# Performance work log

Measured on AMD Instinct MI355X. Metric: run time of the kernel, lower is better.

The kernel has to match this reference:

```python
import jax, jax.numpy as jnp
import numpy as np

B, CIN, H, W = 4, 1024, 64, 64
PLANES = 256
K = 3
DIL = 2
PAD = DIL * (K - 1) // 2  # = 2
EPS = 1e-5


def setup_inputs() -> dict:
    key = jax.random.key(0)
    ks = jax.random.split(key, 16)
    d = {}
    d['x'] = jax.random.normal(ks[0], (B, CIN, H, W), dtype=jnp.float32)
    # conv1: 1x1, inplanes->planes, no bias
    d['w1'] = jax.random.normal(ks[1], (PLANES, CIN), dtype=jnp.float32) * 0.02
    d['gamma1'] = jnp.ones((PLANES,), jnp.float32)
    d['beta1'] = jnp.zeros((PLANES,), jnp.float32)
    d['mean1'] = jax.random.normal(ks[2], (PLANES,), dtype=jnp.float32) * 0.1
    d['var1'] = jax.random.uniform(ks[3], (PLANES,), minval=0.5, maxval=1.5, dtype=jnp.float32)
    # deform_offset: 3x3 conv planes->18, with bias
    d['woff'] = jax.random.normal(ks[4], (18, PLANES, K, K), dtype=jnp.float32) * 0.01
    d['boff'] = jnp.zeros((18,), jnp.float32)
    # conv2 (deformable): 3x3 planes->planes, with bias
    d['w2'] = jax.random.normal(ks[5], (PLANES, PLANES, K, K), dtype=jnp.float32) * 0.02
    d['bconv2'] = jnp.zeros((PLANES,), jnp.float32)
    d['gamma2'] = jnp.ones((PLANES,), jnp.float32)
    d['beta2'] = jnp.zeros((PLANES,), jnp.float32)
    d['mean2'] = jax.random.normal(ks[6], (PLANES,), dtype=jnp.float32) * 0.1
    d['var2'] = jax.random.uniform(ks[7], (PLANES,), minval=0.5, maxval=1.5, dtype=jnp.float32)
    # conv3: 1x1 planes->planes*4, no bias
    d['w3'] = jax.random.normal(ks[8], (PLANES * 4, PLANES), dtype=jnp.float32) * 0.02
    d['gamma3'] = jnp.ones((PLANES * 4,), jnp.float32)
    d['beta3'] = jnp.zeros((PLANES * 4,), jnp.float32)
    d['mean3'] = jax.random.normal(ks[9], (PLANES * 4,), dtype=jnp.float32) * 0.1
    d['var3'] = jax.random.uniform(ks[10], (PLANES * 4,), minval=0.5, maxval=1.5, dtype=jnp.float32)
    return d


def _bn(x, gamma, beta, mean, var):
    # inference-mode BatchNorm over channel dim (NCHW)
    inv = jax.lax.rsqrt(var + EPS)
    return (x - mean[:, None, None]) * (inv * gamma)[:, None, None] + beta[:, None, None]


def _deform_conv(x, offset, w, b):
    # x: [B,C,H,W]; offset: [B,18,H,W] ordered (dy,dx) per kernel tap; w: [O,C,3,3]
    Bn, C, Hh, Ww = x.shape
    off = offset.reshape(Bn, K * K, 2, Hh, Ww)
    off_y, off_x = off[:, :, 0], off[:, :, 1]          # [B,9,H,W]
    kk = jnp.arange(K * K)
    base_y = (kk // K) * DIL - PAD                      # [9]
    base_x = (kk % K) * DIL - PAD
    ys = jnp.arange(Hh, dtype=x.dtype)
    xs = jnp.arange(Ww, dtype=x.dtype)
    py = base_y.astype(x.dtype)[None, :, None, None] + ys[None, None, :, None] + off_y
    px = base_x.astype(x.dtype)[None, :, None, None] + xs[None, None, None, :] + off_x

    def sample_one(img, py1, px1):
        # img [C,H,W]; py1/px1 [9,H,W] -> [C,9,H,W] bilinear with zero padding
        y0 = jnp.floor(py1)
        x0 = jnp.floor(px1)
        wy = py1 - y0
        wx = px1 - x0

        def gather(yc, xc):
            yi = yc.astype(jnp.int32)
            xi = xc.astype(jnp.int32)
            valid = ((yi >= 0) & (yi < Hh) & (xi >= 0) & (xi < Ww)).astype(img.dtype)
            yi = jnp.clip(yi, 0, Hh - 1)
            xi = jnp.clip(xi, 0, Ww - 1)
            return img[:, yi, xi] * valid[None]

        v00 = gather(y0, x0)
        v01 = gather(y0, x0 + 1)
        v10 = gather(y0 + 1, x0)
        v11 = gather(y0 + 1, x0 + 1)
        return (v00 * ((1 - wy) * (1 - wx))[None] + v01 * ((1 - wy) * wx)[None]
                + v10 * (wy * (1 - wx))[None] + v11 * (wy * wx)[None])

    sampled = jax.vmap(sample_one)(x, py, px)           # [B,C,9,H,W]
    out = jnp.einsum('bckhw,ock->bohw', sampled, w.reshape(w.shape[0], C, K * K))
    return out + b[None, :, None, None]


def reference(x, w1, gamma1, beta1, mean1, var1, woff, boff, w2, bconv2,
              gamma2, beta2, mean2, var2, w3, gamma3, beta3, mean3, var3):
    residual = x
    out = jnp.einsum('bchw,oc->bohw', x, w1)            # conv1 1x1
    out = jax.nn.relu(_bn(out, gamma1, beta1, mean1, var1))
    offset = jax.lax.conv_general_dilated(
        out, woff, window_strides=(1, 1), padding=((PAD, PAD), (PAD, PAD)),
        rhs_dilation=(DIL, DIL), dimension_numbers=('NCHW', 'OIHW', 'NCHW'))
    offset = offset + boff[None, :, None, None]
    out = _deform_conv(out, offset, w2, bconv2)
    out = jax.nn.relu(_bn(out, gamma2, beta2, mean2, var2))
    out = jnp.einsum('bchw,oc->bohw', out, w3)          # conv3 1x1
    out = _bn(out, gamma3, beta3, mean3, var3)
    return jax.nn.relu(out + residual)
```

## Files before the change

### kernel.cpp

```cpp
#include <hip/hip_runtime.h>

#define EPS_BN 1e-5f

typedef __bf16 bf16x8 __attribute__((ext_vector_type(8)));
typedef float f32x4 __attribute__((ext_vector_type(4)));

__device__ __forceinline__ unsigned short f2bf(float f) {
  union { float f; unsigned u; } v; v.f = f;
  unsigned r = v.u + 0x7fffu + ((v.u >> 16) & 1u);
  return (unsigned short)(r >> 16);
}
__device__ __forceinline__ float bf2f(unsigned short h) {
  union { unsigned u; float f; } v; v.u = ((unsigned)h) << 16;
  return v.f;
}

__global__ __launch_bounds__(256) void prep_all(
    const float* __restrict__ w1, const float* __restrict__ w2, const float* __restrict__ woff,
    const float* __restrict__ w3,
    const float* g1, const float* b1, const float* m1, const float* v1,
    const float* g2, const float* b2, const float* m2, const float* v2, const float* bconv2,
    const float* g3, const float* b3, const float* m3, const float* v3,
    unsigned short* __restrict__ w1b, unsigned short* __restrict__ w2r,
    uint4* __restrict__ act1Pz, unsigned short* __restrict__ wob,
    unsigned short* __restrict__ w3b, float* __restrict__ shift3,
    float* s1, float* h1, float* s2, float* h2) {
  int bid = blockIdx.x, tid = threadIdx.x;
  if (bid < 1024) {
    int i = bid * 256 + tid;
    w1b[i] = f2bf(w1[i]);
  } else if (bid < 3328) {
    int i = (bid - 1024) * 256 + tid;
    int o = i / 2304, r = i % 2304;
    int kk = r / 256, c = r % 256;
    w2r[i] = f2bf(w2[(size_t)o * 2304 + c * 9 + kk]);
  } else if (bid < 5640) {
    int i = (bid - 3328) * 256 + tid;
    if (i < 591872) act1Pz[i] = uint4{0, 0, 0, 0};
  } else if (bid < 5928) {
    int i = (bid - 5640) * 256 + tid;
    int o = i / 2304, r = i % 2304;
    int kk = r / 256, c = r % 256;
    wob[i] = (o < 18) ? f2bf(woff[(size_t)o * 2304 + c * 9 + kk]) : (unsigned short)0;
  } else if (bid < 6952) {
    int i = (bid - 5928) * 256 + tid;
    int o = i >> 8;
    float sc = rsqrtf(v3[o] + EPS_BN) * g3[o];
    w3b[i] = f2bf(w3[i] * sc);
  } else if (bid < 6956) {
    int c = (bid - 6952) * 256 + tid;
    float sc = rsqrtf(v3[c] + EPS_BN) * g3[c];
    shift3[c] = b3[c] - m3[c] * sc;
  } else {
    int c = tid;
    float sc1 = rsqrtf(v1[c] + EPS_BN) * g1[c];
    s1[c] = sc1; h1[c] = b1[c] - m1[c] * sc1;
    float sc2 = rsqrtf(v2[c] + EPS_BN) * g2[c];
    s2[c] = sc2; h2[c] = b2[c] + (bconv2[c] - m2[c]) * sc2;
  }
}

__global__ __launch_bounds__(256) void transpose_x(const float* __restrict__ x,
                                                   unsigned short* __restrict__ xT) {
  __shared__ float t[32][33];
  int b = blockIdx.z;
  int p0 = blockIdx.x * 32, c0 = blockIdx.y * 32;
  int tx = threadIdx.x & 31, ty = threadIdx.x >> 5;
  const float* xb = x + (size_t)b * 1024 * 4096;
#pragma unroll
  for (int j = 0; j < 4; ++j) {
    int c = c0 + ty + j * 8;
    t[ty + j * 8][tx] = xb[(size_t)c * 4096 + p0 + tx];
  }
  __syncthreads();
  unsigned short* xTb = xT + (size_t)b * 4096 * 1024;
#pragma unroll
  for (int j = 0; j < 4; ++j) {
    int p = p0 + ty + j * 8;
    xTb[(size_t)p * 1024 + c0 + tx] = f2bf(t[tx][ty + j * 8]);
  }
}

__global__ __launch_bounds__(256) void gemm_split(
    const unsigned short* __restrict__ A, const unsigned short* __restrict__ Bm,
    unsigned short* __restrict__ part, int M, int N, int K, int KH) {
  __shared__ unsigned short sA[128 * 32];
  __shared__ unsigned short sB[128 * 32];
  int tid = threadIdx.x, lane = tid & 63, wv = tid >> 6;
  int z = blockIdx.z;
  int m0 = blockIdx.y * 128, n0 = blockIdx.x * 128;
  f32x4 acc[4][4] = {};
  int rowA = tid >> 2;
  int kcol = (tid & 3) * 8;
  int wm = wv & 1, wn = wv >> 1;
  int lane15 = lane & 15, quad8 = (lane >> 4) * 8;
  int kend = z * KH + KH;

  for (int k0 = z * KH; k0 < kend; k0 += 32) {
    __syncthreads();
#pragma unroll
    for (int r = 0; r < 2; ++r) {
      const unsigned short* gp = A + (size_t)(m0 + r * 64 + rowA) * K + k0 + kcol;
      __builtin_amdgcn_global_load_lds((const __attribute__((address_space(1))) void*)gp,
                                       (__attribute__((address_space(3))) void*)&sA[r * 2048 + wv * 512],
                                       16, 0, 0);
    }
#pragma unroll
    for (int r = 0; r < 2; ++r) {
      const unsigned short* gp = Bm + (size_t)(n0 + r * 64 + rowA) * K + k0 + kcol;
      __builtin_amdgcn_global_load_lds((const __attribute__((address_space(1))) void*)gp,
                                       (__attribute__((address_space(3))) void*)&sB[r * 2048 + wv * 512],
                                       16, 0, 0);
    }
    __syncthreads();
    bf16x8 afr[4], bfr[4];
#pragma unroll
    for (int mi = 0; mi < 4; ++mi)
      afr[mi] = *(const bf16x8*)&sA[(wm * 64 + mi * 16 + lane15) * 32 + quad8];
#pragma unroll
    for (int ni = 0; ni < 4; ++ni)
      bfr[ni] = *(const bf16x8*)&sB[(wn * 64 + ni * 16 + lane15) * 32 + quad8];
#pragma unroll
    for (int mi = 0; mi < 4; ++mi)
#pragma unroll
      for (int ni = 0; ni < 4; ++ni)
        acc[mi][ni] = __builtin_amdgcn_mfma_f32_16x16x32_bf16(afr[mi], bfr[ni], acc[mi][ni], 0, 0, 0);
  }

  unsigned short* outH = part + (size_t)z * M * N;
#pragma unroll
  for (int mi = 0; mi < 4; ++mi) {
#pragma unroll
    for (int ni = 0; ni < 4; ++ni) {
      int col = n0 + wn * 64 + ni * 16 + lane15;
#pragma unroll
      for (int reg = 0; reg < 4; ++reg) {
        int row = m0 + wm * 64 + mi * 16 + (lane >> 4) * 4 + reg;
        outH[(size_t)row * N + col] = f2bf(acc[mi][ni][reg]);
      }
    }
  }
}

template <int NS, int PAD>
__global__ __launch_bounds__(256) void epi_bn(const unsigned short* __restrict__ part,
                                              const float* __restrict__ scale,
                                              const float* __restrict__ shift,
                                              unsigned short* __restrict__ outT,
                                              unsigned short* __restrict__ outP) {
  int gid = blockIdx.x * 256 + threadIdx.x;
  int row = gid >> 5, c0 = (gid & 31) * 8;
  float v[8] = {};
#pragma unroll
  for (int s = 0; s < NS; ++s) {
    uint4 q = *(const uint4*)(part + (size_t)s * 16384 * 256 + (size_t)row * 256 + c0);
    unsigned u[4] = {q.x, q.y, q.z, q.w};
#pragma unroll
    for (int j = 0; j < 4; ++j) {
      v[2 * j]     += bf2f((unsigned short)(u[j] & 0xffffu));
      v[2 * j + 1] += bf2f((unsigned short)(u[j] >> 16));
    }
  }
  float sc[8], sh[8];
  *(float4*)&sc[0] = *(const float4*)(scale + c0); *(float4*)&sc[4] = *(const float4*)(scale + c0 + 4);
  *(float4*)&sh[0] = *(const float4*)(shift + c0); *(float4*)&sh[4] = *(const float4*)(shift + c0 + 4);
  unsigned o[4];
#pragma unroll
  for (int j = 0; j < 4; ++j) {
    float lo = fmaxf(v[2 * j] * sc[2 * j] + sh[2 * j], 0.f);
    float hi = fmaxf(v[2 * j + 1] * sc[2 * j + 1] + sh[2 * j + 1], 0.f);
    o[j] = (unsigned)f2bf(lo) | ((unsigned)f2bf(hi) << 16);
  }
  uint4 pk{o[0], o[1], o[2], o[3]};
  *(uint4*)(outT + (size_t)row * 256 + c0) = pk;
  if constexpr (PAD) {
    int bb = row >> 12, p = row & 4095;
    *(uint4*)(outP + (((size_t)(bb * 68) + (p >> 6) + 2) * 68 + (p & 63) + 2) * 256 + c0) = pk;
  }
}

__global__ __launch_bounds__(256) void gemm_res(
    const unsigned short* __restrict__ A, const unsigned short* __restrict__ Bm,
    float* __restrict__ outp, const float* __restrict__ shift3,
    const float* __restrict__ resid, int M, int N, int K, long bStrideB, long bStrideOut) {
  __shared__ unsigned short sA[128 * 32];
  __shared__ unsigned short sB[128 * 32];
  __shared__ float tbuf[32 * 132];
  int tid = threadIdx.x, lane = tid & 63, wv = tid >> 6;
  int z = blockIdx.z;
  const unsigned short* Bz = Bm + (size_t)z * bStrideB;
  int m0 = blockIdx.y * 128, n0 = blockIdx.x * 128;
  f32x4 acc[4][4] = {};
  int rowA = tid >> 2;
  int kcol = (tid & 3) * 8;
  int wm = wv & 1, wn = wv >> 1;
  int lane15 = lane & 15, quad8 = (lane >> 4) * 8, quad = lane >> 4;

  for (int k0 = 0; k0 < K; k0 += 32) {
    __syncthreads();
#pragma unroll
    for (int r = 0; r < 2; ++r) {
      const unsigned short* gp = A + (size_t)(m0 + r * 64 + rowA) * K + k0 + kcol;
      __builtin_amdgcn_global_load_lds((const __attribute__((address_space(1))) void*)gp,
                                       (__attribute__((address_space(3))) void*)&sA[r * 2048 + wv * 512],
                                       16, 0, 0);
    }
#pragma unroll
    for (int r = 0; r < 2; ++r) {
      const unsigned short* gp = Bz + (size_t)(n0 + r * 64 + rowA) * K + k0 + kcol;
      __builtin_amdgcn_global_load_lds((const __attribute__((address_space(1))) void*)gp,
                                       (__attribute__((address_space(3))) void*)&sB[r * 2048 + wv * 512],
                                       16, 0, 0);
    }
    __syncthreads();
    bf16x8 afr[4], bfr[4];
#pragma unroll
    for (int mi = 0; mi < 4; ++mi)
      afr[mi] = *(const bf16x8*)&sA[(wm * 64 + mi * 16 + lane15) * 32 + quad8];
#pragma unroll
    for (int ni = 0; ni < 4; ++ni)
      bfr[ni] = *(const bf16x8*)&sB[(wn * 64 + ni * 16 + lane15) * 32 + quad8];
#pragma unroll
    for (int mi = 0; mi < 4; ++mi)
#pragma unroll
      for (int ni = 0; ni < 4; ++ni)
        acc[mi][ni] = __builtin_amdgcn_mfma_f32_16x16x32_bf16(afr[mi], bfr[ni], acc[mi][ni], 0, 0, 0);
  }

  float* outF = outp + (size_t)z * bStrideOut;
  const float* res = resid + (size_t)z * bStrideOut;
  int trow = tid >> 3;
  int tcol = (tid & 7) * 4;
  int growBase = m0 + (trow >> 4) * 64 + (trow & 15);
#pragma unroll
  for (int mi = 0; mi < 4; ++mi) {
    __syncthreads();
#pragma unroll
    for (int ni = 0; ni < 4; ++ni)
#pragma unroll
      for (int reg = 0; reg < 4; ++reg)
        tbuf[(wm * 16 + quad * 4 + reg) * 132 + wn * 64 + ni * 16 + lane15] = acc[mi][ni][reg];
    __syncthreads();
    int gr = growBase + mi * 16;
    float sh = shift3[gr];
    const float* rp = res + (size_t)gr * N + n0 + tcol;
    float* op = outF + (size_t)gr * N + n0 + tcol;
    const float* lp = &tbuf[trow * 132 + tcol];
#pragma unroll
    for (int j = 0; j < 4; ++j) {
      float4 rv = *(const float4*)(rp + j * 32);
      float4 lv = *(const float4*)(lp + j * 32);
      float4 ov;
      ov.x = fmaxf(lv.x + sh + rv.x, 0.f);
      ov.y = fmaxf(lv.y + sh + rv.y, 0.f);
      ov.z = fmaxf(lv.z + sh + rv.z, 0.f);
      ov.w = fmaxf(lv.w + sh + rv.w, 0.f);
      *(float4*)(op + j * 32) = ov;
    }
  }
}

__global__ __launch_bounds__(256) void off_gemm(const unsigned short* __restrict__ actP,
                                                const unsigned short* __restrict__ wob,
                                                const float* __restrict__ boff,
                                                float* __restrict__ offsP) {
  __shared__ unsigned short sA[64 * 64];
  __shared__ unsigned short sB[32 * 64];
  int tid = threadIdx.x, lane = tid & 63, wv = tid >> 6;
  int m0 = blockIdx.x * 64;
  int lane15 = lane & 15, quad8 = (lane >> 4) * 8;
  int rowA = tid >> 3;
  int kc = (tid & 7) * 8;

  const unsigned short* baseA[2];
#pragma unroll
  for (int r = 0; r < 2; ++r) {
    int row = m0 + r * 32 + rowA;
    int b = row >> 12, p = row & 4095;
    baseA[r] = actP + (((size_t)(b * 68) + (p >> 6) + 2) * 68 + (p & 63) + 2) * 256 + kc;
  }
  const unsigned short* baseB = wob + (size_t)rowA * 2304 + kc;

  f32x4 acc[2] = {};
  for (int kk = 0; kk < 9; ++kk) {
    int shift = ((kk / 3) * 2 - 2) * 68 + ((kk % 3) * 2 - 2);
#pragma unroll 1
    for (int c0 = 0; c0 < 256; c0 += 64) {
      __syncthreads();
#pragma unroll
      for (int r = 0; r < 2; ++r) {
        const unsigned short* gp = baseA[r] + (long)shift * 256 + c0;
        __builtin_amdgcn_global_load_lds((const __attribute__((address_space(1))) void*)gp,
                                         (__attribute__((address_space(3))) void*)&sA[r * 2048 + wv * 512],
                                         16, 0, 0);
      }
      {
        const unsigned short* gp = baseB + kk * 256 + c0;
        __builtin_amdgcn_global_load_lds((const __attribute__((address_space(1))) void*)gp,
                                         (__attribute__((address_space(3))) void*)&sB[wv * 512],
                                         16, 0, 0);
      }
      __syncthreads();
      bf16x8 afr[2], bfr[2][2];
#pragma unroll
      for (int kq = 0; kq < 2; ++kq) {
        afr[kq] = *(const bf16x8*)&sA[(wv * 16 + lane15) * 64 + kq * 32 + quad8];
#pragma unroll
        for (int ni = 0; ni < 2; ++ni)
          bfr[kq][ni] = *(const bf16x8*)&sB[(ni * 16 + lane15) * 64 + kq * 32 + quad8];
      }
#pragma unroll
      for (int kq = 0; kq < 2; ++kq)
#pragma unroll
        for (int ni = 0; ni < 2; ++ni)
          acc[ni] = __builtin_amdgcn_mfma_f32_16x16x32_bf16(afr[kq], bfr[kq][ni], acc[ni], 0, 0, 0);
    }
  }

#pragma unroll
  for (int ni = 0; ni < 2; ++ni) {
    int o = ni * 16 + lane15;
    if (o < 18) {
      float bo = boff[o];
#pragma unroll
      for (int reg = 0; reg < 4; ++reg) {
        int row = m0 + wv * 16 + (lane >> 4) * 4 + reg;
        offsP[(size_t)row * 18 + o] = acc[ni][reg] + bo;
      }
    }
  }
}

__global__ __launch_bounds__(256) void deform_sample(const unsigned short* __restrict__ act1T,
                                                     const float* __restrict__ offsP,
                                                     unsigned short* __restrict__ S) {
  int g = threadIdx.x >> 5, t = threadIdx.x & 31;
  int idx = blockIdx.x * 8 + g;
  int b = idx >> 12, p = idx & 4095;
  int h = p >> 6, w = p & 63;
  const unsigned short* actb = act1T + (size_t)b * 4096 * 256 + t * 8;
  unsigned short* Sp = S + (size_t)idx * 2304 + t * 8;
  float ov = (t < 18) ? offsP[(size_t)idx * 18 + t] : 0.f;
#pragma unroll
  for (int kk = 0; kk < 9; ++kk) {
    float offy = __shfl(ov, 2 * kk, 32);
    float offx = __shfl(ov, 2 * kk + 1, 32);
    float py = (float)(h + (kk / 3) * 2 - 2) + offy;
    float px = (float)(w + (kk % 3) * 2 - 2) + offx;
    float fy = floorf(py), fx = floorf(px);
    int y0 = (int)fy, x0 = (int)fx;
    float wy = py - fy, wx = px - fx;
    bool yv0 = (y0 >= 0 && y0 < 64), yv1 = (y0 >= -1 && y0 < 63);
    bool xv0 = (x0 >= 0 && x0 < 64), xv1 = (x0 >= -1 && x0 < 63);
    const unsigned short* cb = actb + (y0 * 64 + x0) * 256;
    uint4 q00{0,0,0,0}, q01{0,0,0,0}, q10{0,0,0,0}, q11{0,0,0,0};
    if (yv0 && xv0) q00 = *(const uint4*)(cb);
    if (yv0 && xv1) q01 = *(const uint4*)(cb + 256);
    if (yv1 && xv0) q10 = *(const uint4*)(cb + 64 * 256);
    if (yv1 && xv1) q11 = *(const uint4*)(cb + 64 * 256 + 256);
    float w00 = (1.f - wy) * (1.f - wx), w01 = (1.f - wy) * wx;
    float w10 = wy * (1.f - wx), w11 = wy * wx;
    unsigned u00[4] = {q00.x, q00.y, q00.z, q00.w};
    unsigned u01[4] = {q01.x, q01.y, q01.z, q01.w};
    unsigned u10[4] = {q10.x, q10.y, q10.z, q10.w};
    unsigned u11[4] = {q11.x, q11.y, q11.z, q11.w};
    unsigned out[4];
#pragma unroll
    for (int j = 0; j < 4; ++j) {
      float lo = bf2f((unsigned short)(u00[j] & 0xffffu)) * w00 +
                 bf2f((unsigned short)(u01[j] & 0xffffu)) * w01 +
                 bf2f((unsigned short)(u10[j] & 0xffffu)) * w10 +
                 bf2f((unsigned short)(u11[j] & 0xffffu)) * w11;
      float hi = bf2f((unsigned short)(u00[j] >> 16)) * w00 +
                 bf2f((unsigned short)(u01[j] >> 16)) * w01 +
                 bf2f((unsigned short)(u10[j] >> 16)) * w10 +
                 bf2f((unsigned short)(u11[j] >> 16)) * w11;
      out[j] = (unsigned)f2bf(lo) | ((unsigned)f2bf(hi) << 16);
    }
    *(uint4*)(Sp + kk * 256) = uint4{out[0], out[1], out[2], out[3]};
  }
}

extern "C" void kernel_launch(void* const* d_in, const int* in_sizes, int n_in,
                              void* d_out, int out_size, void* d_ws, size_t ws_size,
                              hipStream_t stream) {
  const float* x      = (const float*)d_in[0];
  const float* w1     = (const float*)d_in[1];
  const float* gamma1 = (const float*)d_in[2];
  const float* beta1  = (const float*)d_in[3];
  const float* mean1  = (const float*)d_in[4];
  const float* var1   = (const float*)d_in[5];
  const float* woff   = (const float*)d_in[6];
  const float* boff   = (const float*)d_in[7];
  const float* w2     = (const float*)d_in[8];
  const float* bconv2 = (const float*)d_in[9];
  const float* gamma2 = (const float*)d_in[10];
  const float* beta2  = (const float*)d_in[11];
  const float* mean2  = (const float*)d_in[12];
  const float* var2   = (const float*)d_in[13];
  const float* w3     = (const float*)d_in[14];
  const float* gamma3 = (const float*)d_in[15];
  const float* beta3  = (const float*)d_in[16];
  const float* mean3  = (const float*)d_in[17];
  const float* var3   = (const float*)d_in[18];

  char* ws = (char*)d_ws;
  unsigned short* xT    = (unsigned short*)(ws);
  unsigned short* act1T = (unsigned short*)(ws + 33554432);
  unsigned short* act2T = (unsigned short*)(ws + 41943040);
  unsigned short* S     = (unsigned short*)(ws + 50331648);
  float*          offs  = (float*)(ws + 125829120);
  unsigned short* w1b   = (unsigned short*)(ws + 127008768);
  unsigned short* w2r   = (unsigned short*)(ws + 127533056);
  unsigned short* w3b   = (unsigned short*)(ws + 128712704);
  float*          bnS1  = (float*)(ws + 129236992);
  float*          bnH1  = (float*)(ws + 129238016);
  float*          bnS2  = (float*)(ws + 129239040);
  float*          bnH2  = (float*)(ws + 129240064);
  float*          shift3= (float*)(ws + 129241088);
  unsigned short* act1P = S;
  unsigned short* part1 = (unsigned short*)(ws + 62914560);
  unsigned short* part2 = (unsigned short*)ws;
  unsigned short* wob   = act2T;

  prep_all<<<6957, 256, 0, stream>>>(w1, w2, woff, w3,
                                     gamma1, beta1, mean1, var1,
                                     gamma2, beta2, mean2, var2, bconv2,
                                     gamma3, beta3, mean3, var3,
                                     w1b, w2r, (uint4*)act1P, wob, w3b, shift3,
                                     bnS1, bnH1, bnS2, bnH2);
  transpose_x<<<dim3(128, 32, 4), 256, 0, stream>>>(x, xT);

  gemm_split<<<dim3(2, 128, 4), 256, 0, stream>>>(xT, w1b, part1, 16384, 256, 1024, 256);
  epi_bn<4, 1><<<2048, 256, 0, stream>>>(part1, bnS1, bnH1, act1T, act1P);

  off_gemm<<<256, 256, 0, stream>>>(act1P, wob, boff, offs);
  deform_sample<<<dim3(2048), 256, 0, stream>>>(act1T, offs, S);

  gemm_split<<<dim3(2, 128, 4), 256, 0, stream>>>(S, w2r, part2, 16384, 256, 2304, 576);
  epi_bn<4, 0><<<2048, 256, 0, stream>>>(part2, bnS2, bnH2, act2T, nullptr);

  gemm_res<<<dim3(32, 8, 4), 256, 0, stream>>>(w3b, act2T, (float*)d_out, shift3, x,
                                               1024, 4096, 256, 4096L * 256, 4194304L);
}
```

Baseline: 308.1 us.

## Vectorize transpose and GEMM stores via LDS staging; halve split-K factor

The transpose kernel now writes four packed bf16 values per thread with a single 8-byte store instead of scalar 2-byte stores. The split-K GEMM epilogue stages each 32x128 accumulator slab through a padded shared-memory buffer so each thread writes 16 contiguous bf16 values as two 16-byte stores, replacing scattered 2-byte writes. The split-K factor for both GEMMs drops from 4 to 2, which halves partial-sum traffic and the epilogue reduction but also halves the grid to 512 blocks and adds LDS usage plus extra barriers in the GEMM.

```diff
diff --git a/kernel.cpp b/kernel.cpp
--- a/kernel.cpp
+++ b/kernel.cpp
@@ -74,11 +74,13 @@
   }
   __syncthreads();
   unsigned short* xTb = xT + (size_t)b * 4096 * 1024;
-#pragma unroll
-  for (int j = 0; j < 4; ++j) {
-    int p = p0 + ty + j * 8;
-    xTb[(size_t)p * 1024 + c0 + tx] = f2bf(t[tx][ty + j * 8]);
-  }
+  int pl = threadIdx.x >> 3;
+  int cl = (threadIdx.x & 7) * 4;
+  float v0 = t[cl][pl], v1 = t[cl + 1][pl], v2 = t[cl + 2][pl], v3 = t[cl + 3][pl];
+  uint2 pk;
+  pk.x = (unsigned)f2bf(v0) | ((unsigned)f2bf(v1) << 16);
+  pk.y = (unsigned)f2bf(v2) | ((unsigned)f2bf(v3) << 16);
+  *(uint2*)(xTb + (size_t)(p0 + pl) * 1024 + c0 + cl) = pk;
 }
 
 __global__ __launch_bounds__(256) void gemm_split(
@@ -86,6 +88,7 @@
     unsigned short* __restrict__ part, int M, int N, int K, int KH) {
   __shared__ unsigned short sA[128 * 32];
   __shared__ unsigned short sB[128 * 32];
+  __shared__ float tbuf[32 * 132];
   int tid = threadIdx.x, lane = tid & 63, wv = tid >> 6;
   int z = blockIdx.z;
   int m0 = blockIdx.y * 128, n0 = blockIdx.x * 128;
@@ -93,7 +96,7 @@
   int rowA = tid >> 2;
   int kcol = (tid & 3) * 8;
   int wm = wv & 1, wn = wv >> 1;
-  int lane15 = lane & 15, quad8 = (lane >> 4) * 8;
+  int lane15 = lane & 15, quad8 = (lane >> 4) * 8, quad = lane >> 4;
   int kend = z * KH + KH;
 
   for (int k0 = z * KH; k0 < kend; k0 += 32) {
@@ -128,17 +131,27 @@
   }
 
   unsigned short* outH = part + (size_t)z * M * N;
+  int trow = tid >> 3;
+  int tcol16 = (tid & 7) * 16;
+  int growBase = m0 + (trow >> 4) * 64 + (trow & 15);
 #pragma unroll
   for (int mi = 0; mi < 4; ++mi) {
-#pragma unroll
-    for (int ni = 0; ni < 4; ++ni) {
-      int col = n0 + wn * 64 + ni * 16 + lane15;
-#pragma unroll
-      for (int reg = 0; reg < 4; ++reg) {
-        int row = m0 + wm * 64 + mi * 16 + (lane >> 4) * 4 + reg;
-        outH[(size_t)row * N + col] = f2bf(acc[mi][ni][reg]);
-      }
-    }
+    __syncthreads();
+#pragma unroll
+    for (int ni = 0; ni < 4; ++ni)
+#pragma unroll
+      for (int reg = 0; reg < 4; ++reg)
+        tbuf[(wm * 16 + quad * 4 + reg) * 132 + wn * 64 + ni * 16 + lane15] = acc[mi][ni][reg];
+    __syncthreads();
+    int gr = growBase + mi * 16;
+    const float* lp = &tbuf[trow * 132 + tcol16];
+    unsigned o[8];
+#pragma unroll
+    for (int j = 0; j < 8; ++j)
+      o[j] = (unsigned)f2bf(lp[2 * j]) | ((unsigned)f2bf(lp[2 * j + 1]) << 16);
+    unsigned short* op = outH + (size_t)gr * 256 + n0 + tcol16;
+    *(uint4*)(op) = uint4{o[0], o[1], o[2], o[3]};
+    *(uint4*)(op + 8) = uint4{o[4], o[5], o[6], o[7]};
   }
 }
 
@@ -431,14 +444,14 @@
                                      bnS1, bnH1, bnS2, bnH2);
   transpose_x<<<dim3(128, 32, 4), 256, 0, stream>>>(x, xT);
 
-  gemm_split<<<dim3(2, 128, 4), 256, 0, stream>>>(xT, w1b, part1, 16384, 256, 1024, 256);
-  epi_bn<4, 1><<<2048, 256, 0, stream>>>(part1, bnS1, bnH1, act1T, act1P);
+  gemm_split<<<dim3(2, 128, 2), 256, 0, stream>>>(xT, w1b, part1, 16384, 256, 1024, 512);
+  epi_bn<2, 1><<<2048, 256, 0, stream>>>(part1, bnS1, bnH1, act1T, act1P);
 
   off_gemm<<<256, 256, 0, stream>>>(act1P, wob, boff, offs);
   deform_sample<<<dim3(2048), 256, 0, stream>>>(act1T, offs, S);
 
-  gemm_split<<<dim3(2, 128, 4), 256, 0, stream>>>(S, w2r, part2, 16384, 256, 2304, 576);
-  epi_bn<4, 0><<<2048, 256, 0, stream>>>(part2, bnS2, bnH2, act2T, nullptr);
+  gemm_split<<<dim3(2, 128, 2), 256, 0, stream>>>(S, w2r, part2, 16384, 256, 2304, 1152);
+  epi_bn<2, 0><<<2048, 256, 0, stream>>>(part2, bnS2, bnH2, act2T, nullptr);
 
   gemm_res<<<dim3(32, 8, 4), 256, 0, stream>>>(w3b, act2T, (float*)d_out, shift3, x,
                                                1024, 4096, 256, 4096L * 256, 4194304L);
```

After: 302.5 us. No clear change (-1.8%).
